# Performance work log

Hardware: AMD Instinct MI355X
Metric: run time of the kernel (lower is better)

## Reference

```python
import jax, jax.numpy as jnp
import numpy as np

BLOCK = 32           # sparsity_config.block
STRIDE_BLOCKS = 4    # stride 128 // block 32
B, H, L, HD = 2, 16, 4096, 64


def _make_fixed_layout(nb, bs):
    """DeepSpeed 'fixed' unidirectional layout, numverts=vertsize=1 (same for all heads)."""
    lay = np.zeros((nb, nb), dtype=np.int64)
    # local: lower-triangular within each stride window
    for i in range(0, nb, bs):
        for j in range(i, i + bs):
            lay[j, i:j + 1] = 1
    # global: vertical stripe at column offset bs-1 of every window, causal (col < row)
    start = bs - 1
    for i in range(nb):
        for j in range(start, i, bs):
            lay[i, j] = 1
    rows, cols = np.nonzero(lay)  # sorted by row
    return jnp.asarray(rows, jnp.int32), jnp.asarray(cols, jnp.int32)


def setup_inputs() -> dict:
    key = jax.random.key(0)
    kq, kk, kv = jax.random.split(key, 3)
    query = jax.random.normal(kq, (B, H, L, HD), jnp.float32)
    key_t = jax.random.normal(kk, (B, H, L, HD), jnp.float32)
    value = jax.random.normal(kv, (B, H, L, HD), jnp.float32)
    rows, cols = _make_fixed_layout(L // BLOCK, STRIDE_BLOCKS)
    return {"query": query, "key": key_t, "value": value,
            "rows": rows, "cols": cols, "block": BLOCK}


def reference(query, key, value, rows, cols, block):
    b, h, l, hd = query.shape
    nb = l // block
    scale = float(hd) ** (-0.5)
    # [nb, B, H, block, hd] with block-row axis leading for gather/scatter
    qb = jnp.moveaxis(query.reshape(b, h, nb, block, hd), 2, 0)
    kb = jnp.moveaxis(key.reshape(b, h, nb, block, hd), 2, 0)
    vb = jnp.moveaxis(value.reshape(b, h, nb, block, hd), 2, 0)
    # sdd: scores only on active blocks -> [nnz, B, H, block, block]
    s = jnp.einsum('nbhqd,nbhkd->nbhqk', qb[rows], kb[cols]) * scale
    # block-sparse softmax over each query row (segment reduce over blocks sharing a row)
    m_blk = s.max(-1)  # [nnz, B, H, block]
    row_max = jnp.full((nb, b, h, block), -jnp.inf, s.dtype).at[rows].max(m_blk)
    e = jnp.exp(s - row_max[rows][..., None])
    denom = jnp.zeros((nb, b, h, block), s.dtype).at[rows].add(e.sum(-1))
    p = e / denom[rows][..., None]
    # dsd: probs @ value, scatter-add into block rows
    ob = jnp.zeros((nb, b, h, block, hd), s.dtype).at[rows].add(
        jnp.einsum('nbhqk,nbhkd->nbhqd', p, vb[cols]))
    return jnp.moveaxis(ob, 0, 2).reshape(b, h, l, hd)
```

## Files before the change

kernel.cpp:

```cpp
#include <hip/hip_runtime.h>
#include <math.h>

#define BH    32
#define LSEQ  4096
#define HD    64
#define BLK   32
#define NB    128
#define NWIN  32
#define QSCALE 0.18033688011112042f

#define KSTR 34
#define VSTR 17

typedef _Float16 h2  __attribute__((ext_vector_type(2)));
typedef _Float16 h8  __attribute__((ext_vector_type(8)));
typedef float    f16v __attribute__((ext_vector_type(16)));

static __device__ __forceinline__ h2 pk(float a, float b) {
    return __builtin_bit_cast(h2, __builtin_amdgcn_cvt_pkrtz(a, b));
}
static __device__ __forceinline__ unsigned pku(float a, float b) {
    return __builtin_bit_cast(unsigned, __builtin_amdgcn_cvt_pkrtz(a, b));
}
static __device__ __forceinline__ short h16(float x) {
    return __builtin_bit_cast(short, (_Float16)x);
}
static __device__ __forceinline__ h8 mk8(h2 a, h2 b, h2 c, h2 d) {
    h8 r;
    r[0] = a[0]; r[1] = a[1]; r[2] = b[0]; r[3] = b[1];
    r[4] = c[0]; r[5] = c[1]; r[6] = d[0]; r[7] = d[1];
    return r;
}

__global__ __launch_bounds__(256)
void sparse_attn_pair(const float* __restrict__ Q, const float* __restrict__ K,
                      const float* __restrict__ V, float* __restrict__ out)
{
    const int id = (int)blockIdx.x;
    const int bh = id & 31;
    const int p  = id >> 5;

    const int t    = (int)threadIdx.x;
    const int d    = t >> 6;
    const int lane = t & 63;
    const int l31  = lane & 31;
    const int h    = lane >> 5;

    __shared__ __align__(16) unsigned kbuf[2][BLK * KSTR];
    __shared__ __align__(16) unsigned vbuf[2][HD * VSTR];

    const size_t base = (size_t)bh * (LSEQ * HD);

    const int srow = t >> 3;
    const int sdg  = t & 7;

    const float* kgb = K + base + (size_t)srow * HD + sdg * 8;
    const float* vgb = V + base + (size_t)srow * HD + sdg * 8;

    float4 kA, kB, vA, vB;

    auto loadR = [&](int w, int j) {
        const int col = (j < w) ? (4 * j + 3) : (4 * w + (j - w));
        const size_t off = (size_t)col * (BLK * HD);
        kA = *(const float4*)(kgb + off);
        kB = *(const float4*)(kgb + off + 4);
        vA = *(const float4*)(vgb + off);
        vB = *(const float4*)(vgb + off + 4);
    };
    auto writeL = [&](int b) {
        uint2 w0, w1;
        w0.x = pku(kA.x, kA.y); w0.y = pku(kA.z, kA.w);
        w1.x = pku(kB.x, kB.y); w1.y = pku(kB.z, kB.w);
        *(uint2*)&kbuf[b][srow * KSTR + sdg * 4]     = w0;
        *(uint2*)&kbuf[b][srow * KSTR + sdg * 4 + 2] = w1;
        short* vs = (short*)&vbuf[b][0];
        const int vd0 = sdg * 8;
        vs[(vd0 + 0) * (2 * VSTR) + srow] = h16(vA.x);
        vs[(vd0 + 1) * (2 * VSTR) + srow] = h16(vA.y);
        vs[(vd0 + 2) * (2 * VSTR) + srow] = h16(vA.z);
        vs[(vd0 + 3) * (2 * VSTR) + srow] = h16(vA.w);
        vs[(vd0 + 4) * (2 * VSTR) + srow] = h16(vB.x);
        vs[(vd0 + 5) * (2 * VSTR) + srow] = h16(vB.y);
        vs[(vd0 + 6) * (2 * VSTR) + srow] = h16(vB.z);
        vs[(vd0 + 7) * (2 * VSTR) + srow] = h16(vB.w);
    };

    int pb = 0;
    loadR(p, 0);

    for (int ph = 0; ph < 2; ++ph) {
        const int w = ph ? (31 - p) : p;
        const int r = 4 * w + d;
        const int n = w + 4;

        const float* qp = Q + base + (size_t)(r * BLK + l31) * HD + 8 * h;
        h8 qf[4];
#pragma unroll
        for (int tt = 0; tt < 4; ++tt) {
            float4 a = *(const float4*)(qp + 16 * tt);
            float4 b = *(const float4*)(qp + 16 * tt + 4);
            qf[tt] = mk8(pk(a.x * QSCALE, a.y * QSCALE), pk(a.z * QSCALE, a.w * QSCALE),
                         pk(b.x * QSCALE, b.y * QSCALE), pk(b.z * QSCALE, b.w * QSCALE));
        }

        f16v o0 = {}, o1 = {};
        float2 ls2 = make_float2(0.0f, 0.0f);

        for (int j = 0; j < n; ++j, pb ^= 1) {
            writeL(pb);
            if (j + 1 < n)      loadR(w, j + 1);
            else if (ph == 0)   loadR(31 - p, 0);
            __builtin_amdgcn_s_waitcnt(0xc07f);
            __builtin_amdgcn_s_barrier();

            if (j < w || (j - w) <= d) {
                const unsigned* kb = kbuf[pb];
                const unsigned* vb = vbuf[pb];

                f16v st = {};
#pragma unroll
                for (int tt = 0; tt < 4; ++tt) {
                    const int kw = l31 * KSTR + 8 * tt + 4 * h;
                    uint2 u0 = *(const uint2*)&kb[kw];
                    uint2 u1 = *(const uint2*)&kb[kw + 2];
                    uint4 uu; uu.x = u0.x; uu.y = u0.y; uu.z = u1.x; uu.w = u1.y;
                    h8 kf = __builtin_bit_cast(h8, uu);
                    st = __builtin_amdgcn_mfma_f32_32x32x16_f16(kf, qf[tt], st, 0, 0, 0);
                }

                float ps[16];
#pragma unroll
                for (int g = 0; g < 16; ++g) ps[g] = __builtin_exp2f(st[g]);
#pragma unroll
                for (int g = 0; g < 8; ++g) {
                    ls2.x += ps[2 * g];
                    ls2.y += ps[2 * g + 1];
                }
                h2 ph2[8];
#pragma unroll
                for (int jj = 0; jj < 8; ++jj) ph2[jj] = pk(ps[2 * jj], ps[2 * jj + 1]);

#pragma unroll
                for (int t2 = 0; t2 < 2; ++t2) {
                    h2 s0 = h ? ph2[4 * t2]     : ph2[4 * t2 + 2];
                    h2 s1 = h ? ph2[4 * t2 + 1] : ph2[4 * t2 + 3];
                    int i0 = __shfl_xor(__builtin_bit_cast(int, s0), 32);
                    int i1 = __shfl_xor(__builtin_bit_cast(int, s1), 32);
                    h2 g0 = __builtin_bit_cast(h2, i0), g1 = __builtin_bit_cast(h2, i1);
                    h2 c0 = h ? g0 : ph2[4 * t2];
                    h2 c1 = h ? g1 : ph2[4 * t2 + 1];
                    h2 c2 = h ? ph2[4 * t2 + 2] : g0;
                    h2 c3 = h ? ph2[4 * t2 + 3] : g1;
                    h8 pa = mk8(c0, c1, c2, c3);

                    const int va0 = l31 * VSTR + 8 * t2 + 4 * h;
                    const int va1 = (32 + l31) * VSTR + 8 * t2 + 4 * h;
                    uint4 u0, u1;
                    u0.x = vb[va0]; u0.y = vb[va0 + 1]; u0.z = vb[va0 + 2]; u0.w = vb[va0 + 3];
                    u1.x = vb[va1]; u1.y = vb[va1 + 1]; u1.z = vb[va1 + 2]; u1.w = vb[va1 + 3];
                    h8 vf0 = __builtin_bit_cast(h8, u0);
                    h8 vf1 = __builtin_bit_cast(h8, u1);
                    o0 = __builtin_amdgcn_mfma_f32_32x32x16_f16(pa, vf0, o0, 0, 0, 0);
                    o1 = __builtin_amdgcn_mfma_f32_32x32x16_f16(pa, vf1, o1, 0, 0, 0);
                }
            }
        }

        float lsum = ls2.x + ls2.y;
        lsum += __shfl_xor(lsum, 32);
        const float inv = 1.0f / lsum;

        float* op = out + base + (size_t)(r * BLK) * HD;
#pragma unroll
        for (int g = 0; g < 16; ++g) {
            const int qrow = (g & 3) + 8 * (g >> 2) + 4 * h;
            int iv = __builtin_amdgcn_ds_bpermute(qrow << 2, __float_as_int(inv));
            const float invq = __int_as_float(iv);
            op[(size_t)qrow * HD + l31]      = o0[g] * invq;
            op[(size_t)qrow * HD + 32 + l31] = o1[g] * invq;
        }
    }
}

extern "C" void kernel_launch(void* const* d_in, const int* in_sizes, int n_in,
                              void* d_out, int out_size, void* d_ws, size_t ws_size,
                              hipStream_t stream) {
    const float* Q = (const float*)d_in[0];
    const float* K = (const float*)d_in[1];
    const float* V = (const float*)d_in[2];

    dim3 grid(NWIN * BH / 2);
    dim3 block(256);
    sparse_attn_pair<<<grid, block, 0, stream>>>(Q, K, V, (float*)d_out);
}
```

Baseline: 165.5 us.

## Process two K/V blocks per barrier with both query windows held in registers

The kernel now loads both windows' query fragments up front and treats the combined 39 K/V column blocks as one stream. It stages two blocks per step in a four-slot shared buffer, which halves the number of barriers and interleaves two independent MFMA chains for more instruction-level parallelism. Blocks that a warp should skip are masked to a large negative score instead of branched around, so some wasted MFMA and exp work is traded for uniform control flow. It also requests two blocks per CU via launch bounds, which may constrain register allocation given the larger live state.

```diff
diff --git a/kernel.cpp b/kernel.cpp
--- a/kernel.cpp
+++ b/kernel.cpp
@@ -32,9 +32,9 @@
     return r;
 }
 
-__global__ __launch_bounds__(256)
-void sparse_attn_pair(const float* __restrict__ Q, const float* __restrict__ K,
-                      const float* __restrict__ V, float* __restrict__ out)
+__global__ __launch_bounds__(256, 2)
+void sparse_attn_pair2(const float* __restrict__ Q, const float* __restrict__ K,
+                       const float* __restrict__ V, float* __restrict__ out)
 {
     const int id = (int)blockIdx.x;
     const int bh = id & 31;
@@ -46,10 +46,36 @@
     const int l31  = lane & 31;
     const int h    = lane >> 5;
 
-    __shared__ __align__(16) unsigned kbuf[2][BLK * KSTR];
-    __shared__ __align__(16) unsigned vbuf[2][HD * VSTR];
+    __shared__ __align__(16) unsigned kbuf[4][BLK * KSTR];
+    __shared__ __align__(16) unsigned vbuf[4][HD * VSTR];
 
     const size_t base = (size_t)bh * (LSEQ * HD);
+
+    const int wA = p, wB = 31 - p;
+    const int nA = wA + 4;
+    const int ntot = 39;
+    const int rA = 4 * wA + d, rB = 4 * wB + d;
+
+    h8 qfA[4], qfB[4];
+    {
+        const float* qpA = Q + base + (size_t)(rA * BLK + l31) * HD + 8 * h;
+        const float* qpB = Q + base + (size_t)(rB * BLK + l31) * HD + 8 * h;
+#pragma unroll
+        for (int tt = 0; tt < 4; ++tt) {
+            float4 a = *(const float4*)(qpA + 16 * tt);
+            float4 b = *(const float4*)(qpA + 16 * tt + 4);
+            qfA[tt] = mk8(pk(a.x * QSCALE, a.y * QSCALE), pk(a.z * QSCALE, a.w * QSCALE),
+                          pk(b.x * QSCALE, b.y * QSCALE), pk(b.z * QSCALE, b.w * QSCALE));
+            float4 c = *(const float4*)(qpB + 16 * tt);
+            float4 e = *(const float4*)(qpB + 16 * tt + 4);
+            qfB[tt] = mk8(pk(c.x * QSCALE, c.y * QSCALE), pk(c.z * QSCALE, c.w * QSCALE),
+                          pk(e.x * QSCALE, e.y * QSCALE), pk(e.z * QSCALE, e.w * QSCALE));
+        }
+    }
+
+    f16v oA0 = {}, oA1 = {}, oB0 = {}, oB1 = {};
+    float2 lsA = make_float2(0.0f, 0.0f);
+    float2 lsB = make_float2(0.0f, 0.0f);
 
     const int srow = t >> 3;
     const int sdg  = t & 7;
@@ -57,23 +83,35 @@
     const float* kgb = K + base + (size_t)srow * HD + sdg * 8;
     const float* vgb = V + base + (size_t)srow * HD + sdg * 8;
 
-    float4 kA, kB, vA, vB;
-
-    auto loadR = [&](int w, int j) {
-        const int col = (j < w) ? (4 * j + 3) : (4 * w + (j - w));
-        const size_t off = (size_t)col * (BLK * HD);
-        kA = *(const float4*)(kgb + off);
-        kB = *(const float4*)(kgb + off + 4);
-        vA = *(const float4*)(vgb + off);
-        vB = *(const float4*)(vgb + off + 4);
-    };
-    auto writeL = [&](int b) {
+    float4 k0A, k0B, v0A, v0B, k1A, k1B, v1A, v1B;
+
+    auto colOf = [&](int b) -> int {
+        if (b < nA) return (b < wA) ? (4 * b + 3) : (4 * wA + (b - wA));
+        const int j = b - nA;
+        return (j < wB) ? (4 * j + 3) : (4 * wB + (j - wB));
+    };
+    auto loadS0 = [&](int b) {
+        const size_t off = (size_t)colOf(b) * (BLK * HD);
+        k0A = *(const float4*)(kgb + off);
+        k0B = *(const float4*)(kgb + off + 4);
+        v0A = *(const float4*)(vgb + off);
+        v0B = *(const float4*)(vgb + off + 4);
+    };
+    auto loadS1 = [&](int b) {
+        const size_t off = (size_t)colOf(b) * (BLK * HD);
+        k1A = *(const float4*)(kgb + off);
+        k1B = *(const float4*)(kgb + off + 4);
+        v1A = *(const float4*)(vgb + off);
+        v1B = *(const float4*)(vgb + off + 4);
+    };
+    auto writeSlot = [&](int bi, const float4& kA, const float4& kB,
+                         const float4& vA, const float4& vB) {
         uint2 w0, w1;
         w0.x = pku(kA.x, kA.y); w0.y = pku(kA.z, kA.w);
         w1.x = pku(kB.x, kB.y); w1.y = pku(kB.z, kB.w);
-        *(uint2*)&kbuf[b][srow * KSTR + sdg * 4]     = w0;
-        *(uint2*)&kbuf[b][srow * KSTR + sdg * 4 + 2] = w1;
-        short* vs = (short*)&vbuf[b][0];
+        *(uint2*)&kbuf[bi][srow * KSTR + sdg * 4]     = w0;
+        *(uint2*)&kbuf[bi][srow * KSTR + sdg * 4 + 2] = w1;
+        short* vs = (short*)&vbuf[bi][0];
         const int vd0 = sdg * 8;
         vs[(vd0 + 0) * (2 * VSTR) + srow] = h16(vA.x);
         vs[(vd0 + 1) * (2 * VSTR) + srow] = h16(vA.y);
@@ -85,91 +123,175 @@
         vs[(vd0 + 7) * (2 * VSTR) + srow] = h16(vB.w);
     };
 
-    int pb = 0;
-    loadR(p, 0);
-
-    for (int ph = 0; ph < 2; ++ph) {
-        const int w = ph ? (31 - p) : p;
-        const int r = 4 * w + d;
-        const int n = w + 4;
-
-        const float* qp = Q + base + (size_t)(r * BLK + l31) * HD + 8 * h;
-        h8 qf[4];
+    auto fused = [&](const h8 (&qf0)[4], const h8 (&qf1)[4],
+                     f16v& o00, f16v& o01, f16v& o10, f16v& o11,
+                     float2& ls0, float2& ls1, bool act0, bool act1,
+                     const unsigned* kb0, const unsigned* vb0,
+                     const unsigned* kb1, const unsigned* vb1) {
+        f16v st0 = {}, st1 = {};
 #pragma unroll
         for (int tt = 0; tt < 4; ++tt) {
-            float4 a = *(const float4*)(qp + 16 * tt);
-            float4 b = *(const float4*)(qp + 16 * tt + 4);
-            qf[tt] = mk8(pk(a.x * QSCALE, a.y * QSCALE), pk(a.z * QSCALE, a.w * QSCALE),
-                         pk(b.x * QSCALE, b.y * QSCALE), pk(b.z * QSCALE, b.w * QSCALE));
-        }
-
-        f16v o0 = {}, o1 = {};
-        float2 ls2 = make_float2(0.0f, 0.0f);
-
-        for (int j = 0; j < n; ++j, pb ^= 1) {
-            writeL(pb);
-            if (j + 1 < n)      loadR(w, j + 1);
-            else if (ph == 0)   loadR(31 - p, 0);
-            __builtin_amdgcn_s_waitcnt(0xc07f);
-            __builtin_amdgcn_s_barrier();
-
-            if (j < w || (j - w) <= d) {
-                const unsigned* kb = kbuf[pb];
-                const unsigned* vb = vbuf[pb];
-
-                f16v st = {};
-#pragma unroll
-                for (int tt = 0; tt < 4; ++tt) {
-                    const int kw = l31 * KSTR + 8 * tt + 4 * h;
-                    uint2 u0 = *(const uint2*)&kb[kw];
-                    uint2 u1 = *(const uint2*)&kb[kw + 2];
-                    uint4 uu; uu.x = u0.x; uu.y = u0.y; uu.z = u1.x; uu.w = u1.y;
-                    h8 kf = __builtin_bit_cast(h8, uu);
-                    st = __builtin_amdgcn_mfma_f32_32x32x16_f16(kf, qf[tt], st, 0, 0, 0);
-                }
-
-                float ps[16];
-#pragma unroll
-                for (int g = 0; g < 16; ++g) ps[g] = __builtin_exp2f(st[g]);
-#pragma unroll
-                for (int g = 0; g < 8; ++g) {
-                    ls2.x += ps[2 * g];
-                    ls2.y += ps[2 * g + 1];
-                }
-                h2 ph2[8];
-#pragma unroll
-                for (int jj = 0; jj < 8; ++jj) ph2[jj] = pk(ps[2 * jj], ps[2 * jj + 1]);
-
-#pragma unroll
-                for (int t2 = 0; t2 < 2; ++t2) {
-                    h2 s0 = h ? ph2[4 * t2]     : ph2[4 * t2 + 2];
-                    h2 s1 = h ? ph2[4 * t2 + 1] : ph2[4 * t2 + 3];
-                    int i0 = __shfl_xor(__builtin_bit_cast(int, s0), 32);
-                    int i1 = __shfl_xor(__builtin_bit_cast(int, s1), 32);
-                    h2 g0 = __builtin_bit_cast(h2, i0), g1 = __builtin_bit_cast(h2, i1);
-                    h2 c0 = h ? g0 : ph2[4 * t2];
-                    h2 c1 = h ? g1 : ph2[4 * t2 + 1];
-                    h2 c2 = h ? ph2[4 * t2 + 2] : g0;
-                    h2 c3 = h ? ph2[4 * t2 + 3] : g1;
-                    h8 pa = mk8(c0, c1, c2, c3);
-
-                    const int va0 = l31 * VSTR + 8 * t2 + 4 * h;
-                    const int va1 = (32 + l31) * VSTR + 8 * t2 + 4 * h;
-                    uint4 u0, u1;
-                    u0.x = vb[va0]; u0.y = vb[va0 + 1]; u0.z = vb[va0 + 2]; u0.w = vb[va0 + 3];
-                    u1.x = vb[va1]; u1.y = vb[va1 + 1]; u1.z = vb[va1 + 2]; u1.w = vb[va1 + 3];
-                    h8 vf0 = __builtin_bit_cast(h8, u0);
-                    h8 vf1 = __builtin_bit_cast(h8, u1);
-                    o0 = __builtin_amdgcn_mfma_f32_32x32x16_f16(pa, vf0, o0, 0, 0, 0);
-                    o1 = __builtin_amdgcn_mfma_f32_32x32x16_f16(pa, vf1, o1, 0, 0, 0);
-                }
-            }
-        }
-
-        float lsum = ls2.x + ls2.y;
+            const int kw = l31 * KSTR + 8 * tt + 4 * h;
+            uint2 a0 = *(const uint2*)&kb0[kw];
+            uint2 a1 = *(const uint2*)&kb0[kw + 2];
+            uint2 b0 = *(const uint2*)&kb1[kw];
+            uint2 b1 = *(const uint2*)&kb1[kw + 2];
+            uint4 ua; ua.x = a0.x; ua.y = a0.y; ua.z = a1.x; ua.w = a1.y;
+            uint4 ub; ub.x = b0.x; ub.y = b0.y; ub.z = b1.x; ub.w = b1.y;
+            st0 = __builtin_amdgcn_mfma_f32_32x32x16_f16(__builtin_bit_cast(h8, ua),
+                                                         qf0[tt], st0, 0, 0, 0);
+            st1 = __builtin_amdgcn_mfma_f32_32x32x16_f16(__builtin_bit_cast(h8, ub),
+                                                         qf1[tt], st1, 0, 0, 0);
+        }
+        const float NEG = -1e30f;
+#pragma unroll
+        for (int g = 0; g < 16; ++g) {
+            st0[g] = act0 ? st0[g] : NEG;
+            st1[g] = act1 ? st1[g] : NEG;
+        }
+        h2 ph0[8], ph1[8];
+        float sx0 = 0.f, sy0 = 0.f, sx1 = 0.f, sy1 = 0.f;
+#pragma unroll
+        for (int g = 0; g < 8; ++g) {
+            float p00 = __builtin_exp2f(st0[2 * g]);
+            float p01 = __builtin_exp2f(st0[2 * g + 1]);
+            float p10 = __builtin_exp2f(st1[2 * g]);
+            float p11 = __builtin_exp2f(st1[2 * g + 1]);
+            sx0 += p00; sy0 += p01; sx1 += p10; sy1 += p11;
+            ph0[g] = pk(p00, p01);
+            ph1[g] = pk(p10, p11);
+        }
+        ls0.x += sx0; ls0.y += sy0;
+        ls1.x += sx1; ls1.y += sy1;
+#pragma unroll
+        for (int t2 = 0; t2 < 2; ++t2) {
+            h2 s00 = h ? ph0[4 * t2]     : ph0[4 * t2 + 2];
+            h2 s01 = h ? ph0[4 * t2 + 1] : ph0[4 * t2 + 3];
+            h2 s10 = h ? ph1[4 * t2]     : ph1[4 * t2 + 2];
+            h2 s11 = h ? ph1[4 * t2 + 1] : ph1[4 * t2 + 3];
+            int i00 = __shfl_xor(__builtin_bit_cast(int, s00), 32);
+            int i01 = __shfl_xor(__builtin_bit_cast(int, s01), 32);
+            int i10 = __shfl_xor(__builtin_bit_cast(int, s10), 32);
+            int i11 = __shfl_xor(__builtin_bit_cast(int, s11), 32);
+            h2 g00 = __builtin_bit_cast(h2, i00), g01 = __builtin_bit_cast(h2, i01);
+            h2 g10 = __builtin_bit_cast(h2, i10), g11 = __builtin_bit_cast(h2, i11);
+            h2 c00 = h ? g00 : ph0[4 * t2];
+            h2 c01 = h ? g01 : ph0[4 * t2 + 1];
+            h2 c02 = h ? ph0[4 * t2 + 2] : g00;
+            h2 c03 = h ? ph0[4 * t2 + 3] : g01;
+            h2 c10 = h ? g10 : ph1[4 * t2];
+            h2 c11 = h ? g11 : ph1[4 * t2 + 1];
+            h2 c12 = h ? ph1[4 * t2 + 2] : g10;
+            h2 c13 = h ? ph1[4 * t2 + 3] : g11;
+            h8 pa0 = mk8(c00, c01, c02, c03);
+            h8 pa1 = mk8(c10, c11, c12, c13);
+
+            const int va0 = l31 * VSTR + 8 * t2 + 4 * h;
+            const int va1 = (32 + l31) * VSTR + 8 * t2 + 4 * h;
+            uint4 u00, u01, u10, u11;
+            u00.x = vb0[va0]; u00.y = vb0[va0 + 1]; u00.z = vb0[va0 + 2]; u00.w = vb0[va0 + 3];
+            u01.x = vb0[va1]; u01.y = vb0[va1 + 1]; u01.z = vb0[va1 + 2]; u01.w = vb0[va1 + 3];
+            u10.x = vb1[va0]; u10.y = vb1[va0 + 1]; u10.z = vb1[va0 + 2]; u10.w = vb1[va0 + 3];
+            u11.x = vb1[va1]; u11.y = vb1[va1 + 1]; u11.z = vb1[va1 + 2]; u11.w = vb1[va1 + 3];
+            o00 = __builtin_amdgcn_mfma_f32_32x32x16_f16(pa0, __builtin_bit_cast(h8, u00), o00, 0, 0, 0);
+            o01 = __builtin_amdgcn_mfma_f32_32x32x16_f16(pa0, __builtin_bit_cast(h8, u01), o01, 0, 0, 0);
+            o10 = __builtin_amdgcn_mfma_f32_32x32x16_f16(pa1, __builtin_bit_cast(h8, u10), o10, 0, 0, 0);
+            o11 = __builtin_amdgcn_mfma_f32_32x32x16_f16(pa1, __builtin_bit_cast(h8, u11), o11, 0, 0, 0);
+        }
+    };
+
+    auto single = [&](const h8 (&qf)[4], f16v& o0, f16v& o1, float2& ls,
+                      const unsigned* kb, const unsigned* vb) {
+        f16v st = {};
+#pragma unroll
+        for (int tt = 0; tt < 4; ++tt) {
+            const int kw = l31 * KSTR + 8 * tt + 4 * h;
+            uint2 u0 = *(const uint2*)&kb[kw];
+            uint2 u1 = *(const uint2*)&kb[kw + 2];
+            uint4 uu; uu.x = u0.x; uu.y = u0.y; uu.z = u1.x; uu.w = u1.y;
+            st = __builtin_amdgcn_mfma_f32_32x32x16_f16(__builtin_bit_cast(h8, uu),
+                                                        qf[tt], st, 0, 0, 0);
+        }
+        h2 ph2[8];
+        float sx = 0.f, sy = 0.f;
+#pragma unroll
+        for (int g = 0; g < 8; ++g) {
+            float p0 = __builtin_exp2f(st[2 * g]);
+            float p1 = __builtin_exp2f(st[2 * g + 1]);
+            sx += p0; sy += p1;
+            ph2[g] = pk(p0, p1);
+        }
+        ls.x += sx; ls.y += sy;
+#pragma unroll
+        for (int t2 = 0; t2 < 2; ++t2) {
+            h2 s0 = h ? ph2[4 * t2]     : ph2[4 * t2 + 2];
+            h2 s1 = h ? ph2[4 * t2 + 1] : ph2[4 * t2 + 3];
+            int i0 = __shfl_xor(__builtin_bit_cast(int, s0), 32);
+            int i1 = __shfl_xor(__builtin_bit_cast(int, s1), 32);
+            h2 g0 = __builtin_bit_cast(h2, i0), g1 = __builtin_bit_cast(h2, i1);
+            h2 c0 = h ? g0 : ph2[4 * t2];
+            h2 c1 = h ? g1 : ph2[4 * t2 + 1];
+            h2 c2 = h ? ph2[4 * t2 + 2] : g0;
+            h2 c3 = h ? ph2[4 * t2 + 3] : g1;
+            h8 pa = mk8(c0, c1, c2, c3);
+            const int va0 = l31 * VSTR + 8 * t2 + 4 * h;
+            const int va1 = (32 + l31) * VSTR + 8 * t2 + 4 * h;
+            uint4 u0, u1;
+            u0.x = vb[va0]; u0.y = vb[va0 + 1]; u0.z = vb[va0 + 2]; u0.w = vb[va0 + 3];
+            u1.x = vb[va1]; u1.y = vb[va1 + 1]; u1.z = vb[va1 + 2]; u1.w = vb[va1 + 3];
+            o0 = __builtin_amdgcn_mfma_f32_32x32x16_f16(pa, __builtin_bit_cast(h8, u0), o0, 0, 0, 0);
+            o1 = __builtin_amdgcn_mfma_f32_32x32x16_f16(pa, __builtin_bit_cast(h8, u1), o1, 0, 0, 0);
+        }
+    };
+
+    loadS0(0);
+    loadS1(1);
+
+    for (int bb = 0; bb + 1 < ntot; bb += 2) {
+        const int par = (bb >> 1) & 1;
+        writeSlot(2 * par + 0, k0A, k0B, v0A, v0B);
+        writeSlot(2 * par + 1, k1A, k1B, v1A, v1B);
+        if (bb + 2 < ntot) {
+            loadS0(bb + 2);
+            if (bb + 3 < ntot) loadS1(bb + 3);
+        }
+        __builtin_amdgcn_s_waitcnt(0xc07f);
+        __builtin_amdgcn_s_barrier();
+
+        const unsigned* kb0 = kbuf[2 * par + 0];
+        const unsigned* vb0 = vbuf[2 * par + 0];
+        const unsigned* kb1 = kbuf[2 * par + 1];
+        const unsigned* vb1 = vbuf[2 * par + 1];
+
+        const bool pB0 = (bb >= nA);
+        const bool pB1 = (bb + 1 >= nA);
+        const int j0 = pB0 ? (bb - nA) : bb;
+        const int j1 = pB1 ? (bb + 1 - nA) : (bb + 1);
+        const int w0 = pB0 ? wB : wA;
+        const int w1 = pB1 ? wB : wA;
+        const bool act0 = (j0 < w0) || ((j0 - w0) <= d);
+        const bool act1 = (j1 < w1) || ((j1 - w1) <= d);
+
+        if (!pB1) {
+            fused(qfA, qfA, oA0, oA1, oA0, oA1, lsA, lsA, act0, act1, kb0, vb0, kb1, vb1);
+        } else if (pB0) {
+            fused(qfB, qfB, oB0, oB1, oB0, oB1, lsB, lsB, act0, act1, kb0, vb0, kb1, vb1);
+        } else {
+            fused(qfA, qfB, oA0, oA1, oB0, oB1, lsA, lsB, act0, act1, kb0, vb0, kb1, vb1);
+        }
+    }
+
+    {
+        writeSlot(2, k0A, k0B, v0A, v0B);
+        __builtin_amdgcn_s_waitcnt(0xc07f);
+        __builtin_amdgcn_s_barrier();
+        if (d == 3) single(qfB, oB0, oB1, lsB, kbuf[2], vbuf[2]);
+    }
+
+    auto finish = [&](float2 ls, const f16v& o0, const f16v& o1, int r) {
+        float lsum = ls.x + ls.y;
         lsum += __shfl_xor(lsum, 32);
         const float inv = 1.0f / lsum;
-
         float* op = out + base + (size_t)(r * BLK) * HD;
 #pragma unroll
         for (int g = 0; g < 16; ++g) {
@@ -179,7 +301,9 @@
             op[(size_t)qrow * HD + l31]      = o0[g] * invq;
             op[(size_t)qrow * HD + 32 + l31] = o1[g] * invq;
         }
-    }
+    };
+    finish(lsA, oA0, oA1, rA);
+    finish(lsB, oB0, oB1, rB);
 }
 
 extern "C" void kernel_launch(void* const* d_in, const int* in_sizes, int n_in,
@@ -191,5 +315,5 @@
 
     dim3 grid(NWIN * BH / 2);
     dim3 block(256);
-    sparse_attn_pair<<<grid, block, 0, stream>>>(Q, K, V, (float*)d_out);
-}
+    sparse_attn_pair2<<<grid, block, 0, stream>>>(Q, K, V, (float*)d_out);
+}
```

New measurement: 166.5 us. No clear change (+0.6%).

## Load V fragments directly from global memory into registers, bypassing LDS

Applied to the files above, without the earlier changes.

V is no longer staged through shared memory with a transposed fp16 layout. Each wave now reads the V elements its MFMA B-operand needs straight from global memory into registers, with scalar strided loads, and converts them to fp16 just before the PV MFMA. This removes the LDS transpose stores and the V LDS reads, and halves shared memory use. In exchange it issues 32 uncoalesced-per-row scalar global loads per active block per thread. Those loads are not double-buffered, so global latency is exposed right before use, and four waves redundantly reload the same V tile.

```diff
diff --git a/kernel.cpp b/kernel.cpp
--- a/kernel.cpp
+++ b/kernel.cpp
@@ -10,7 +10,6 @@
 #define QSCALE 0.18033688011112042f
 
 #define KSTR 34
-#define VSTR 17
 
 typedef _Float16 h2  __attribute__((ext_vector_type(2)));
 typedef _Float16 h8  __attribute__((ext_vector_type(8)));
@@ -22,9 +21,6 @@
 static __device__ __forceinline__ unsigned pku(float a, float b) {
     return __builtin_bit_cast(unsigned, __builtin_amdgcn_cvt_pkrtz(a, b));
 }
-static __device__ __forceinline__ short h16(float x) {
-    return __builtin_bit_cast(short, (_Float16)x);
-}
 static __device__ __forceinline__ h8 mk8(h2 a, h2 b, h2 c, h2 d) {
     h8 r;
     r[0] = a[0]; r[1] = a[1]; r[2] = b[0]; r[3] = b[1];
@@ -33,7 +29,7 @@
 }
 
 __global__ __launch_bounds__(256)
-void sparse_attn_pair(const float* __restrict__ Q, const float* __restrict__ K,
+void sparse_attn_vreg(const float* __restrict__ Q, const float* __restrict__ K,
                       const float* __restrict__ V, float* __restrict__ out)
 {
     const int id = (int)blockIdx.x;
@@ -47,7 +43,6 @@
     const int h    = lane >> 5;
 
     __shared__ __align__(16) unsigned kbuf[2][BLK * KSTR];
-    __shared__ __align__(16) unsigned vbuf[2][HD * VSTR];
 
     const size_t base = (size_t)bh * (LSEQ * HD);
 
@@ -55,38 +50,26 @@
     const int sdg  = t & 7;
 
     const float* kgb = K + base + (size_t)srow * HD + sdg * 8;
-    const float* vgb = V + base + (size_t)srow * HD + sdg * 8;
 
-    float4 kA, kB, vA, vB;
+    float4 kA, kB;
+    float vr0[16], vr1[16];
 
-    auto loadR = [&](int w, int j) {
+    auto loadK = [&](int w, int j) {
         const int col = (j < w) ? (4 * j + 3) : (4 * w + (j - w));
         const size_t off = (size_t)col * (BLK * HD);
         kA = *(const float4*)(kgb + off);
         kB = *(const float4*)(kgb + off + 4);
-        vA = *(const float4*)(vgb + off);
-        vB = *(const float4*)(vgb + off + 4);
     };
-    auto writeL = [&](int b) {
+    auto writeK = [&](int b) {
         uint2 w0, w1;
         w0.x = pku(kA.x, kA.y); w0.y = pku(kA.z, kA.w);
         w1.x = pku(kB.x, kB.y); w1.y = pku(kB.z, kB.w);
         *(uint2*)&kbuf[b][srow * KSTR + sdg * 4]     = w0;
         *(uint2*)&kbuf[b][srow * KSTR + sdg * 4 + 2] = w1;
-        short* vs = (short*)&vbuf[b][0];
-        const int vd0 = sdg * 8;
-        vs[(vd0 + 0) * (2 * VSTR) + srow] = h16(vA.x);
-        vs[(vd0 + 1) * (2 * VSTR) + srow] = h16(vA.y);
-        vs[(vd0 + 2) * (2 * VSTR) + srow] = h16(vA.z);
-        vs[(vd0 + 3) * (2 * VSTR) + srow] = h16(vA.w);
-        vs[(vd0 + 4) * (2 * VSTR) + srow] = h16(vB.x);
-        vs[(vd0 + 5) * (2 * VSTR) + srow] = h16(vB.y);
-        vs[(vd0 + 6) * (2 * VSTR) + srow] = h16(vB.z);
-        vs[(vd0 + 7) * (2 * VSTR) + srow] = h16(vB.w);
     };
 
     int pb = 0;
-    loadR(p, 0);
+    loadK(p, 0);
 
     for (int ph = 0; ph < 2; ++ph) {
         const int w = ph ? (31 - p) : p;
@@ -107,15 +90,28 @@
         float2 ls2 = make_float2(0.0f, 0.0f);
 
         for (int j = 0; j < n; ++j, pb ^= 1) {
-            writeL(pb);
-            if (j + 1 < n)      loadR(w, j + 1);
-            else if (ph == 0)   loadR(31 - p, 0);
+            const bool act = (j < w) || ((j - w) <= d);
+
+            if (act) {
+                const int col = (j < w) ? (4 * j + 3) : (4 * w + (j - w));
+                const float* vp = V + base + (size_t)(col * BLK + 8 * h) * HD + l31;
+#pragma unroll
+                for (int t2 = 0; t2 < 2; ++t2)
+#pragma unroll
+                    for (int e = 0; e < 8; ++e) {
+                        vr0[8 * t2 + e] = vp[(size_t)(16 * t2 + e) * HD];
+                        vr1[8 * t2 + e] = vp[(size_t)(16 * t2 + e) * HD + 32];
+                    }
+            }
+
+            writeK(pb);
+            if (j + 1 < n)      loadK(w, j + 1);
+            else if (ph == 0)   loadK(31 - p, 0);
             __builtin_amdgcn_s_waitcnt(0xc07f);
             __builtin_amdgcn_s_barrier();
 
-            if (j < w || (j - w) <= d) {
+            if (act) {
                 const unsigned* kb = kbuf[pb];
-                const unsigned* vb = vbuf[pb];
 
                 f16v st = {};
 #pragma unroll
@@ -153,13 +149,12 @@
                     h2 c3 = h ? ph2[4 * t2 + 3] : g1;
                     h8 pa = mk8(c0, c1, c2, c3);
 
-                    const int va0 = l31 * VSTR + 8 * t2 + 4 * h;
-                    const int va1 = (32 + l31) * VSTR + 8 * t2 + 4 * h;
-                    uint4 u0, u1;
-                    u0.x = vb[va0]; u0.y = vb[va0 + 1]; u0.z = vb[va0 + 2]; u0.w = vb[va0 + 3];
-                    u1.x = vb[va1]; u1.y = vb[va1 + 1]; u1.z = vb[va1 + 2]; u1.w = vb[va1 + 3];
-                    h8 vf0 = __builtin_bit_cast(h8, u0);
-                    h8 vf1 = __builtin_bit_cast(h8, u1);
+                    h8 vf0, vf1;
+#pragma unroll
+                    for (int e = 0; e < 8; ++e) {
+                        vf0[e] = (_Float16)vr0[8 * t2 + e];
+                        vf1[e] = (_Float16)vr1[8 * t2 + e];
+                    }
                     o0 = __builtin_amdgcn_mfma_f32_32x32x16_f16(pa, vf0, o0, 0, 0, 0);
                     o1 = __builtin_amdgcn_mfma_f32_32x32x16_f16(pa, vf1, o1, 0, 0, 0);
                 }
@@ -191,5 +186,5 @@
 
     dim3 grid(NWIN * BH / 2);
     dim3 block(256);
-    sparse_attn_pair<<<grid, block, 0, stream>>>(Q, K, V, (float*)d_out);
+    sparse_attn_vreg<<<grid, block, 0, stream>>>(Q, K, V, (float*)d_out);
 }
```

Measured after the change: 206.0 us. 1.25x slower.

## Split key blocks across two wave groups and combine partial outputs in LDS

Applied to the files above, without the earlier changes.

Blocks grow to 512 threads, forming two groups of four waves. Each group handles alternate key/value blocks of the window (even or odd j) with its own double-buffered LDS, and the partial outputs and row sums are merged through shared memory before the normalised write. The aim is to halve the serial loop length per block and raise wave-level parallelism and latency hiding. In exchange it adds an LDS reduction with extra barriers and larger shared memory. The V stride also changes from 17 to 18 so V fragments can be read as 64-bit loads.

```diff
diff --git a/kernel.cpp b/kernel.cpp
--- a/kernel.cpp
+++ b/kernel.cpp
@@ -10,7 +10,8 @@
 #define QSCALE 0.18033688011112042f
 
 #define KSTR 34
-#define VSTR 17
+#define VSTR 18
+#define GWORDS (BLK * KSTR + HD * VSTR)
 
 typedef _Float16 h2  __attribute__((ext_vector_type(2)));
 typedef _Float16 h8  __attribute__((ext_vector_type(8)));
@@ -32,66 +33,83 @@
     return r;
 }
 
-__global__ __launch_bounds__(256)
-void sparse_attn_pair(const float* __restrict__ Q, const float* __restrict__ K,
-                      const float* __restrict__ V, float* __restrict__ out)
+__global__ __launch_bounds__(512, 4)
+void sparse_attn_ks(const float* __restrict__ Q, const float* __restrict__ K,
+                    const float* __restrict__ V, float* __restrict__ out)
 {
     const int id = (int)blockIdx.x;
     const int bh = id & 31;
     const int p  = id >> 5;
 
     const int t    = (int)threadIdx.x;
-    const int d    = t >> 6;
+    const int wv   = t >> 6;
+    const int g    = wv >> 2;
+    const int d    = wv & 3;
     const int lane = t & 63;
     const int l31  = lane & 31;
     const int h    = lane >> 5;
 
-    __shared__ __align__(16) unsigned kbuf[2][BLK * KSTR];
-    __shared__ __align__(16) unsigned vbuf[2][HD * VSTR];
+    __shared__ __align__(16) unsigned smem[2][2][GWORDS];
 
     const size_t base = (size_t)bh * (LSEQ * HD);
 
-    const int srow = t >> 3;
-    const int sdg  = t & 7;
+    const int wA = p, wB = 31 - p;
+    const int nA = wA + 4, nB = wB + 4;
+
+    const int t4   = t & 255;
+    const int srow = t4 >> 3;
+    const int sdg  = t4 & 7;
 
     const float* kgb = K + base + (size_t)srow * HD + sdg * 8;
     const float* vgb = V + base + (size_t)srow * HD + sdg * 8;
 
-    float4 kA, kB, vA, vB;
-
-    auto loadR = [&](int w, int j) {
-        const int col = (j < w) ? (4 * j + 3) : (4 * w + (j - w));
-        const size_t off = (size_t)col * (BLK * HD);
-        kA = *(const float4*)(kgb + off);
-        kB = *(const float4*)(kgb + off + 4);
-        vA = *(const float4*)(vgb + off);
-        vB = *(const float4*)(vgb + off + 4);
+    float4 kA_, kB_, vA_, vB_;
+
+    const int LA   = (nA - g + 1) >> 1;
+    const int LB   = (nB - g + 1) >> 1;
+    const int Ltot = LA + LB;
+
+    auto colFlat = [&](int idx) -> int {
+        int w, j;
+        if (idx < LA) { w = wA; j = 2 * idx + g; }
+        else          { w = wB; j = 2 * (idx - LA) + g; }
+        return (j < w) ? (4 * j + 3) : (4 * w + (j - w));
     };
-    auto writeL = [&](int b) {
+    auto loadKV = [&](int idx) {
+        const size_t off = (size_t)colFlat(idx) * (BLK * HD);
+        kA_ = *(const float4*)(kgb + off);
+        kB_ = *(const float4*)(kgb + off + 4);
+        vA_ = *(const float4*)(vgb + off);
+        vB_ = *(const float4*)(vgb + off + 4);
+    };
+    auto writeKV = [&](int b) {
+        unsigned* kb = &smem[g][b][0];
         uint2 w0, w1;
-        w0.x = pku(kA.x, kA.y); w0.y = pku(kA.z, kA.w);
-        w1.x = pku(kB.x, kB.y); w1.y = pku(kB.z, kB.w);
-        *(uint2*)&kbuf[b][srow * KSTR + sdg * 4]     = w0;
-        *(uint2*)&kbuf[b][srow * KSTR + sdg * 4 + 2] = w1;
-        short* vs = (short*)&vbuf[b][0];
+        w0.x = pku(kA_.x, kA_.y); w0.y = pku(kA_.z, kA_.w);
+        w1.x = pku(kB_.x, kB_.y); w1.y = pku(kB_.z, kB_.w);
+        *(uint2*)&kb[srow * KSTR + sdg * 4]     = w0;
+        *(uint2*)&kb[srow * KSTR + sdg * 4 + 2] = w1;
+        short* vs = (short*)&smem[g][b][BLK * KSTR];
         const int vd0 = sdg * 8;
-        vs[(vd0 + 0) * (2 * VSTR) + srow] = h16(vA.x);
-        vs[(vd0 + 1) * (2 * VSTR) + srow] = h16(vA.y);
-        vs[(vd0 + 2) * (2 * VSTR) + srow] = h16(vA.z);
-        vs[(vd0 + 3) * (2 * VSTR) + srow] = h16(vA.w);
-        vs[(vd0 + 4) * (2 * VSTR) + srow] = h16(vB.x);
-        vs[(vd0 + 5) * (2 * VSTR) + srow] = h16(vB.y);
-        vs[(vd0 + 6) * (2 * VSTR) + srow] = h16(vB.z);
-        vs[(vd0 + 7) * (2 * VSTR) + srow] = h16(vB.w);
+        vs[(vd0 + 0) * (2 * VSTR) + srow] = h16(vA_.x);
+        vs[(vd0 + 1) * (2 * VSTR) + srow] = h16(vA_.y);
+        vs[(vd0 + 2) * (2 * VSTR) + srow] = h16(vA_.z);
+        vs[(vd0 + 3) * (2 * VSTR) + srow] = h16(vA_.w);
+        vs[(vd0 + 4) * (2 * VSTR) + srow] = h16(vB_.x);
+        vs[(vd0 + 5) * (2 * VSTR) + srow] = h16(vB_.y);
+        vs[(vd0 + 6) * (2 * VSTR) + srow] = h16(vB_.z);
+        vs[(vd0 + 7) * (2 * VSTR) + srow] = h16(vB_.w);
     };
 
-    int pb = 0;
-    loadR(p, 0);
+    int pb  = 0;
+    int cur = 0;
+    loadKV(0);
 
     for (int ph = 0; ph < 2; ++ph) {
-        const int w = ph ? (31 - p) : p;
+        const int w = ph ? wB : wA;
+        const int n = ph ? nB : nA;
+        const int T = (n + 1) >> 1;
         const int r = 4 * w + d;
-        const int n = w + 4;
 
         const float* qp = Q + base + (size_t)(r * BLK + l31) * HD + 8 * h;
         h8 qf[4];
@@ -106,16 +124,20 @@
         f16v o0 = {}, o1 = {};
         float2 ls2 = make_float2(0.0f, 0.0f);
 
-        for (int j = 0; j < n; ++j, pb ^= 1) {
-            writeL(pb);
-            if (j + 1 < n)      loadR(w, j + 1);
-            else if (ph == 0)   loadR(31 - p, 0);
+        for (int i = 0; i < T; ++i) {
+            const int  j    = 2 * i + g;
+            const bool have = (j < n);
+            if (have) {
+                writeKV(pb);
+                ++cur;
+                if (cur < Ltot) loadKV(cur);
+            }
             __builtin_amdgcn_s_waitcnt(0xc07f);
             __builtin_amdgcn_s_barrier();
 
-            if (j < w || (j - w) <= d) {
-                const unsigned* kb = kbuf[pb];
-                const unsigned* vb = vbuf[pb];
+            if (have && ((j < w) || ((j - w) <= d))) {
+                const unsigned* kb = &smem[g][pb][0];
+                const unsigned* vb = &smem[g][pb][BLK * KSTR];
 
                 f16v st = {};
 #pragma unroll
@@ -130,11 +152,11 @@
 
                 float ps[16];
 #pragma unroll
-                for (int g = 0; g < 16; ++g) ps[g] = __builtin_exp2f(st[g]);
-#pragma unroll
-                for (int g = 0; g < 8; ++g) {
-                    ls2.x += ps[2 * g];
-                    ls2.y += ps[2 * g + 1];
+                for (int gg = 0; gg < 16; ++gg) ps[gg] = __builtin_exp2f(st[gg]);
+#pragma unroll
+                for (int gg = 0; gg < 8; ++gg) {
+                    ls2.x += ps[2 * gg];
+                    ls2.y += ps[2 * gg + 1];
                 }
                 h2 ph2[8];
 #pragma unroll
@@ -155,30 +177,54 @@
 
                     const int va0 = l31 * VSTR + 8 * t2 + 4 * h;
                     const int va1 = (32 + l31) * VSTR + 8 * t2 + 4 * h;
-                    uint4 u0, u1;
-                    u0.x = vb[va0]; u0.y = vb[va0 + 1]; u0.z = vb[va0 + 2]; u0.w = vb[va0 + 3];
-                    u1.x = vb[va1]; u1.y = vb[va1 + 1]; u1.z = vb[va1 + 2]; u1.w = vb[va1 + 3];
+                    uint2 q0 = *(const uint2*)&vb[va0];
+                    uint2 q1 = *(const uint2*)&vb[va0 + 2];
+                    uint2 q2 = *(const uint2*)&vb[va1];
+                    uint2 q3 = *(const uint2*)&vb[va1 + 2];
+                    uint4 u0; u0.x = q0.x; u0.y = q0.y; u0.z = q1.x; u0.w = q1.y;
+                    uint4 u1; u1.x = q2.x; u1.y = q2.y; u1.z = q3.x; u1.w = q3.y;
                     h8 vf0 = __builtin_bit_cast(h8, u0);
                     h8 vf1 = __builtin_bit_cast(h8, u1);
                     o0 = __builtin_amdgcn_mfma_f32_32x32x16_f16(pa, vf0, o0, 0, 0, 0);
                     o1 = __builtin_amdgcn_mfma_f32_32x32x16_f16(pa, vf1, o1, 0, 0, 0);
                 }
             }
+            if (have) pb ^= 1;
         }
 
         float lsum = ls2.x + ls2.y;
         lsum += __shfl_xor(lsum, 32);
-        const float inv = 1.0f / lsum;
-
-        float* op = out + base + (size_t)(r * BLK) * HD;
-#pragma unroll
-        for (int g = 0; g < 16; ++g) {
-            const int qrow = (g & 3) + 8 * (g >> 2) + 4 * h;
-            int iv = __builtin_amdgcn_ds_bpermute(qrow << 2, __float_as_int(inv));
-            const float invq = __int_as_float(iv);
-            op[(size_t)qrow * HD + l31]      = o0[g] * invq;
-            op[(size_t)qrow * HD + 32 + l31] = o1[g] * invq;
-        }
+
+        float* comb = (float*)&smem[0][0][0];
+        __builtin_amdgcn_s_waitcnt(0xc07f);
+        __builtin_amdgcn_s_barrier();
+        if (g == 1) {
+            float* po = comb + (size_t)(d * 64 + lane) * 32;
+#pragma unroll
+            for (int e = 0; e < 16; ++e) { po[e] = o0[e]; po[16 + e] = o1[e]; }
+            comb[8192 + d * 64 + lane] = lsum;
+        }
+        __builtin_amdgcn_s_waitcnt(0xc07f);
+        __builtin_amdgcn_s_barrier();
+        if (g == 0) {
+            const float* po = comb + (size_t)(d * 64 + lane) * 32;
+            const float pls = comb[8192 + d * 64 + lane];
+#pragma unroll
+            for (int e = 0; e < 16; ++e) { o0[e] += po[e]; o1[e] += po[16 + e]; }
+            const float inv = 1.0f / (lsum + pls);
+
+            float* op = out + base + (size_t)(r * BLK) * HD;
+#pragma unroll
+            for (int gg = 0; gg < 16; ++gg) {
+                const int qrow = (gg & 3) + 8 * (gg >> 2) + 4 * h;
+                int iv = __builtin_amdgcn_ds_bpermute(qrow << 2, __float_as_int(inv));
+                const float invq = __int_as_float(iv);
+                op[(size_t)qrow * HD + l31]      = o0[gg] * invq;
+                op[(size_t)qrow * HD + 32 + l31] = o1[gg] * invq;
+            }
+        }
+        __builtin_amdgcn_s_waitcnt(0xc07f);
+        __builtin_amdgcn_s_barrier();
     }
 }
 
@@ -190,6 +236,6 @@
     const float* V = (const float*)d_in[2];
 
     dim3 grid(NWIN * BH / 2);
-    dim3 block(256);
-    sparse_attn_pair<<<grid, block, 0, stream>>>(Q, K, V, (float*)d_out);
-}
+    dim3 block(512);
+    sparse_attn_ks<<<grid, block, 0, stream>>>(Q, K, V, (float*)d_out);
+}
```

Result: slower. 190.2 us (+14.9%).
